# Performance work log

Hardware: AMD Instinct MI355X
Metric: run time of the kernel (lower is better)

The kernel has to match this reference:

```python
import jax, jax.numpy as jnp
import numpy as np
from jax import lax

D_VOCAB = 262
D_EMB = 128
CONV_W = 5
PAD = CONV_W // 2  # 2


def setup_inputs() -> dict:
    key = jax.random.key(0)
    k1, k2, k3, k4, k5 = jax.random.split(key, 5)
    B, W, C = 128, 256, 16
    input = jax.random.randint(k1, (B, W, C), 0, D_VOCAB, dtype=jnp.int64)
    lengths = jax.random.randint(k2, (B, W), 1, C + 1, dtype=jnp.int64)
    # torch init: Embedding weight ~ N(0,1) then *0.1
    emb_weight = jax.random.normal(k3, (D_VOCAB, D_EMB), dtype=jnp.float32) * 0.1
    fan_in = D_EMB * CONV_W
    bound = 1.0 / np.sqrt(fan_in)
    conv_w = jax.random.uniform(k4, (D_EMB, D_EMB, CONV_W), dtype=jnp.float32, minval=-bound, maxval=bound)
    conv_b = jax.random.uniform(k5, (D_EMB,), dtype=jnp.float32, minval=-bound, maxval=bound)
    return {"input": input, "lengths": lengths, "emb_weight": emb_weight,
            "conv_w": conv_w, "conv_b": conv_b}


def reference(input, lengths, emb_weight, conv_w, conv_b):
    B, W, C = input.shape
    ids = input.reshape(B * W, C)                      # [N, C]
    embed = emb_weight[ids]                            # [N, C, E] gather
    x = jnp.transpose(embed, (0, 2, 1))                # [N, E, C] (NCW)
    y = lax.conv_general_dilated(
        x, conv_w,
        window_strides=(1,), padding=[(PAD, PAD)],
        dimension_numbers=("NCH", "OIH", "NCH"))       # [N, E, C]
    y = y + conv_b[None, :, None]
    out = jnp.max(y, axis=-1)                          # max-pool over chars
    return out.reshape(B, W, -1)                       # [B, W, E]
```

## Files before the change

### kernel.cpp

```cpp
#include <hip/hip_runtime.h>
#include <hip/hip_fp16.h>

#define D_VOCAB 262
#define D_EMB   128
#define KW      5
#define NCHAR   16
#define NKO     (KW * D_EMB)

typedef _Float16 h2 __attribute__((ext_vector_type(2)));
typedef _Float16 h8 __attribute__((ext_vector_type(8)));


__global__ __launch_bounds__(256) void transpose_w_kernel(
    const float* __restrict__ cw, float* __restrict__ Wt2) {
  const int gid = blockIdx.x * 256 + threadIdx.x;
  const float val = cw[gid];
  const int o = gid / 640;
  const int r = gid - o * 640;
  const int i = r / 5;
  const int k = r - i * 5;
  Wt2[i * NKO + k * D_EMB + o] = val;
}

__global__ __launch_bounds__(128) void compute_P_kernel(
    const float* __restrict__ emb, const float* __restrict__ Wt2,
    __half* __restrict__ P) {
  __shared__ float emb_s[D_EMB];
  const int b = blockIdx.x;
  const int v = b / KW;
  const int k = b - v * KW;
  const int t = threadIdx.x;
  emb_s[t] = emb[v * D_EMB + t];
  __syncthreads();

  const float* col = Wt2 + k * D_EMB + t;
  float acc = 0.f;
#pragma unroll 16
  for (int i = 0; i < D_EMB; ++i) {
    acc += emb_s[i] * col[i * NKO];
  }
  P[v * NKO + k * D_EMB + t] = __float2half(acc);
}

__global__ __launch_bounds__(256) void conv_char_main_kernel(
    const int* __restrict__ ids, const _Float16* __restrict__ P,
    const float* __restrict__ bias, float* __restrict__ out) {
  const int lane = threadIdx.x & 63;
  const int wave = (int)((blockIdx.x * 256 + threadIdx.x) >> 6);
  const int seq0 = wave << 2;
  const int t    = lane & 15;
  const int grp  = lane >> 4;

  const int myid = ids[seq0 * NCHAR + lane];

  h8 win[5];
#pragma unroll
  for (int w = 0; w < 5; ++w) win[w] = (h8)(_Float16)0.f;
  h8 vmax = (h8)(_Float16)(-60000.f);

  const _Float16* Pl = P + t * 8;

#pragma unroll
  for (int j = 0; j < NCHAR; ++j) {
    const int idj = __shfl(myid, (lane & 48) | j);
    const _Float16* row = Pl + idj * NKO;
#pragma unroll
    for (int k = 0; k < KW; ++k) {
      const int c = j + 2 - k;
      if (c >= 0 && c < NCHAR) {
        const h8 val = *(const h8*)(row + k * D_EMB);
        win[c % 5] += val;
      }
    }
    if (j >= 2) {
      const int w = (j - 2) % 5;
      vmax = __builtin_elementwise_max(vmax, win[w]);
      win[w] = (h8)(_Float16)0.f;
    }
  }
  vmax = __builtin_elementwise_max(vmax, win[14 % 5]);
  vmax = __builtin_elementwise_max(vmax, win[15 % 5]);

  const int o = t * 8;
  const float4 b0 = *(const float4*)(bias + o);
  const float4 b1 = *(const float4*)(bias + o + 4);
  float* op = out + (size_t)(seq0 + grp) * D_EMB + o;
  float4 r0, r1;
  r0.x = (float)vmax[0] + b0.x;
  r0.y = (float)vmax[1] + b0.y;
  r0.z = (float)vmax[2] + b0.z;
  r0.w = (float)vmax[3] + b0.w;
  r1.x = (float)vmax[4] + b1.x;
  r1.y = (float)vmax[5] + b1.y;
  r1.z = (float)vmax[6] + b1.z;
  r1.w = (float)vmax[7] + b1.w;
  *(float4*)op = r0;
  *(float4*)(op + 4) = r1;
}

extern "C" void kernel_launch(void* const* d_in, const int* in_sizes, int n_in,
                              void* d_out, int out_size, void* d_ws, size_t ws_size,
                              hipStream_t stream) {
  const int*   input = (const int*)d_in[0];
  const float* emb   = (const float*)d_in[2];
  const float* cw    = (const float*)d_in[3];
  const float* cb    = (const float*)d_in[4];
  float* out = (float*)d_out;

  _Float16* P   = (_Float16*)d_ws;
  float*    Wt2 = (float*)((char*)d_ws + 335872);

  const int n_seq = in_sizes[0] / NCHAR;

  transpose_w_kernel<<<320, 256, 0, stream>>>(cw, Wt2);
  compute_P_kernel<<<D_VOCAB * KW, 128, 0, stream>>>(emb, Wt2, (__half*)P);

  const int blocks = n_seq / 16;
  conv_char_main_kernel<<<blocks, 256, 0, stream>>>(input, P, cb, out);
}
```

Baseline: 94.36 us.

## Stage per-channel-slice P table in LDS and split channels across blocks

Each block now loads a 16-channel slice of the precomputed P table for all vocab entries and taps into padded shared memory. The per-character gathers then hit LDS instead of global/L2 memory. Sequences are spread across waves with 2 threads per sequence, and ids are loaded with vector loads. In exchange, ids are re-read once per channel slice, each block pays an LDS fill cost, and the large blocks and LDS footprint may limit occupancy.

```diff
diff --git a/kernel.cpp b/kernel.cpp
--- a/kernel.cpp
+++ b/kernel.cpp
@@ -42,33 +42,61 @@
   P[v * NKO + k * D_EMB + t] = __float2half(acc);
 }
 
-__global__ __launch_bounds__(256) void conv_char_main_kernel(
+#define CH       16
+#define NQ       (D_EMB / CH)
+#define VSTRIDE  176
+#define LDS_SZ   (D_VOCAB * VSTRIDE)
+#define SEQ_PER_BLOCK 512
+
+__global__ __launch_bounds__(1024) void conv_char_main_kernel(
     const int* __restrict__ ids, const _Float16* __restrict__ P,
     const float* __restrict__ bias, float* __restrict__ out) {
-  const int lane = threadIdx.x & 63;
-  const int wave = (int)((blockIdx.x * 256 + threadIdx.x) >> 6);
-  const int seq0 = wave << 2;
-  const int t    = lane & 15;
-  const int grp  = lane >> 4;
+  __shared__ __attribute__((aligned(16))) char Plds[LDS_SZ];
 
-  const int myid = ids[seq0 * NCHAR + lane];
+  const int tid  = threadIdx.x;
+  const int lane = tid & 63;
+  const int wid  = tid >> 6;
+  const int q    = blockIdx.x >> 6;
+  const int sb   = blockIdx.x & 63;
+
+#pragma unroll
+  for (int u = tid; u < LDS_SZ / 16; u += 1024) {
+    const int L = u * 16;
+    const int v = L / VSTRIDE;
+    const int r = L - v * VSTRIDE;
+    if (r < 160) {
+      const h8 val = *(const h8*)(P + v * NKO + (r >> 5) * D_EMB + q * CH + ((r & 31) >> 1));
+      *(h8*)(Plds + L) = val;
+    }
+  }
+  __syncthreads();
+
+  const int grp = lane >> 1;
+  const int t   = lane & 1;
+  const int waveSeq0 = sb * SEQ_PER_BLOCK + wid * 32;
+
+  const int4* idp = (const int4*)(ids + waveSeq0 * NCHAR + lane * 8);
+  const int4 idA = idp[0];
+  const int4 idB = idp[1];
 
   h8 win[5];
 #pragma unroll
   for (int w = 0; w < 5; ++w) win[w] = (h8)(_Float16)0.f;
   h8 vmax = (h8)(_Float16)(-60000.f);
 
-  const _Float16* Pl = P + t * 8;
+  const char* Pl = Plds + t * 16;
 
 #pragma unroll
   for (int j = 0; j < NCHAR; ++j) {
-    const int idj = __shfl(myid, (lane & 48) | j);
-    const _Float16* row = Pl + idj * NKO;
+    const int idv = ((j & 7) < 4) ? ((const int*)&idA)[j & 3]
+                                  : ((const int*)&idB)[j & 3];
+    const int idj = __shfl(idv, (lane & 62) | (j >> 3));
+    const char* row = Pl + idj * VSTRIDE;
 #pragma unroll
     for (int k = 0; k < KW; ++k) {
       const int c = j + 2 - k;
       if (c >= 0 && c < NCHAR) {
-        const h8 val = *(const h8*)(row + k * D_EMB);
+        const h8 val = *(const h8*)(row + k * 32);
         win[c % 5] += val;
       }
     }
@@ -81,10 +109,11 @@
   vmax = __builtin_elementwise_max(vmax, win[14 % 5]);
   vmax = __builtin_elementwise_max(vmax, win[15 % 5]);
 
-  const int o = t * 8;
+  const int seq = waveSeq0 + grp;
+  const int o = q * CH + t * 8;
   const float4 b0 = *(const float4*)(bias + o);
   const float4 b1 = *(const float4*)(bias + o + 4);
-  float* op = out + (size_t)(seq0 + grp) * D_EMB + o;
+  float* op = out + (size_t)seq * D_EMB + o;
   float4 r0, r1;
   r0.x = (float)vmax[0] + b0.x;
   r0.y = (float)vmax[1] + b0.y;
@@ -115,6 +144,6 @@
   transpose_w_kernel<<<320, 256, 0, stream>>>(cw, Wt2);
   compute_P_kernel<<<D_VOCAB * KW, 128, 0, stream>>>(emb, Wt2, (__half*)P);
 
-  const int blocks = n_seq / 16;
-  conv_char_main_kernel<<<blocks, 256, 0, stream>>>(input, P, cb, out);
+  const int nsb = n_seq / SEQ_PER_BLOCK;
+  conv_char_main_kernel<<<NQ * nsb, 1024, 0, stream>>>(input, P, cb, out);
 }
```

After: 92.76 us. Within noise of the previous version (-1.7%).
